# Kernel optimization log

Measured on AMD Instinct MI355X. Metric: run time of the kernel, lower is better.

The kernel has to match this reference:

```python
import jax, jax.numpy as jnp
import numpy as np

LATENT = 32
GRID = 32
G1 = GRID + 1  # 33 samples per axis (align_corners grid)
HID = 128
N_POINTS = 1048576


def _trilinear_sample(emb, points):
    """Faithful F.grid_sample(mode='bilinear', padding_mode='zeros', align_corners=True).
    emb: [(G1)^3, C] flat table; points: [n,3] in [-1,1], (x,y,z) -> (W,H,D)."""
    C = emb.shape[1]
    # torch .view(1, C, D, H, W) on the flat [(G1)^3 * C] buffer: same reshape here.
    vol = emb.reshape(C, G1, G1, G1).transpose(1, 2, 3, 0)  # [D, H, W, C]
    # align_corners=True: u in [-1,1] -> pixel coord (u+1)/2 * (size-1)
    coords = (points + 1.0) * (0.5 * (G1 - 1))
    x, y, z = coords[:, 0], coords[:, 1], coords[:, 2]
    x0 = jnp.floor(x); y0 = jnp.floor(y); z0 = jnp.floor(z)
    fx = x - x0; fy = y - y0; fz = z - z0
    x0i = x0.astype(jnp.int32); y0i = y0.astype(jnp.int32); z0i = z0.astype(jnp.int32)
    x1i = x0i + 1; y1i = y0i + 1; z1i = z0i + 1

    def corner(zi, yi, xi, w):
        valid = ((zi >= 0) & (zi < G1) & (yi >= 0) & (yi < G1)
                 & (xi >= 0) & (xi < G1))
        zc = jnp.clip(zi, 0, G1 - 1)
        yc = jnp.clip(yi, 0, G1 - 1)
        xc = jnp.clip(xi, 0, G1 - 1)
        v = vol[zc, yc, xc]  # [n, C] gather
        return v * (w * valid.astype(w.dtype))[:, None]

    wx0, wx1 = 1.0 - fx, fx
    wy0, wy1 = 1.0 - fy, fy
    wz0, wz1 = 1.0 - fz, fz
    lat = (corner(z0i, y0i, x0i, wz0 * wy0 * wx0)
           + corner(z0i, y0i, x1i, wz0 * wy0 * wx1)
           + corner(z0i, y1i, x0i, wz0 * wy1 * wx0)
           + corner(z0i, y1i, x1i, wz0 * wy1 * wx1)
           + corner(z1i, y0i, x0i, wz1 * wy0 * wx0)
           + corner(z1i, y0i, x1i, wz1 * wy0 * wx1)
           + corner(z1i, y1i, x0i, wz1 * wy1 * wx0)
           + corner(z1i, y1i, x1i, wz1 * wy1 * wx1))
    return lat  # [n, C]


def setup_inputs() -> dict:
    key = jax.random.key(0)
    ks = jax.random.split(key, 8)
    points = jax.random.uniform(ks[0], (N_POINTS, 3), dtype=jnp.float32)  # in [0,1) subset of [-1,1]
    emb = jax.random.normal(ks[1], (G1 ** 3, LATENT), dtype=jnp.float32)
    w1 = jax.random.normal(ks[2], (LATENT, HID), dtype=jnp.float32) * 0.05
    b1 = jax.random.normal(ks[3], (HID,), dtype=jnp.float32) * 0.05
    w2 = jax.random.normal(ks[4], (HID, HID), dtype=jnp.float32) * 0.05
    b2 = jax.random.normal(ks[5], (HID,), dtype=jnp.float32) * 0.05
    w3 = jax.random.normal(ks[6], (HID, 1), dtype=jnp.float32) * 0.05
    b3 = jax.random.normal(ks[7], (1,), dtype=jnp.float32) * 0.05
    return {"points": points, "emb": emb, "w1": w1, "b1": b1,
            "w2": w2, "b2": b2, "w3": w3, "b3": b3}


def reference(points, emb, w1, b1, w2, b2, w3, b3):
    lat = _trilinear_sample(emb, points)                # [n, latent]
    h = jax.nn.relu(lat @ w1 + b1)                      # [n, hid]
    h = jax.nn.relu(h @ w2 + b2)                        # [n, hid]
    sdf = jnp.tanh(h @ w3 + b3)                         # [n, 1]
    return sdf
```

## Files before the change

### kernel.cpp

```cpp
#include <hip/hip_runtime.h>
#include <hip/hip_bf16.h>

#define NPTS 1048576
#define G1I  33
#define NV   35937
#define NC   32
#define HIDD 128

typedef _Float16 h8  __attribute__((ext_vector_type(8)));
typedef _Float16 h4  __attribute__((ext_vector_type(4)));
typedef __fp16   p2  __attribute__((ext_vector_type(2)));
typedef float    f4  __attribute__((ext_vector_type(4)));

#define AS_GLOBAL(p) ((const __attribute__((address_space(1))) char*)(p))
#define AS_LDS(p)    ((__attribute__((address_space(3))) char*)(p))

#define WS_A1  0
#define WS_A2  8192
#define WS_EMB 65536
#define WS_NEED (WS_EMB + NV*NC*2)


__global__ __launch_bounds__(256) void vox_prep(
    const float* __restrict__ emb, const float* __restrict__ w1,
    const float* __restrict__ w2, char* __restrict__ ws)
{
    __shared__ _Float16 tile[256][NC];
    const int b = blockIdx.x, t = threadIdx.x;
    _Float16* embh = (_Float16*)(ws + WS_EMB);
    if (b < 141) {
        const int v = b*256 + t;
        #pragma unroll
        for (int c = 0; c < NC; ++c) {
            float val = (v < NV) ? emb[c*NV + v] : 0.f;
            tile[t][c] = (_Float16)val;
        }
        __syncthreads();
        if (v < NV) {
            uint4* dst = (uint4*)(embh + v*NC);
            const uint4* src = (const uint4*)&tile[t][0];
            #pragma unroll
            for (int j = 0; j < 4; ++j) dst[j] = src[j];
        }
    } else if (b < 149) {
        const int t2 = b - 141;
        const int ks = t >> 6, l = t & 63;
        const int gq = l >> 4, colh = l & 15;
        _Float16* a2f = (_Float16*)(ws + WS_A2);
        h8 fr;
        #pragma unroll
        for (int i = 0; i < 8; ++i) {
            const int k = 32*ks + 16*(i>>2) + 4*gq + (i&3);
            fr[i] = (_Float16)w2[k*HIDD + 16*t2 + colh];
        }
        *(h8*)(a2f + ((t2*4+ks)*64 + l)*8) = fr;
    } else {
        _Float16* a1f = (_Float16*)(ws + WS_A1);
        #pragma unroll
        for (int it = 0; it < 2; ++it) {
            const int item = t + it*256;
            const int t8 = item >> 6, l = item & 63;
            const int gq = l >> 4, colh = l & 15;
            h8 fr;
            #pragma unroll
            for (int i = 0; i < 8; ++i) {
                const int k = 16*(i>>2) + 4*gq + (i&3);
                fr[i] = (_Float16)w1[k*HIDD + 16*t8 + colh];
            }
            *(h8*)(a1f + (t8*64 + l)*8) = fr;
        }
    }
}

__global__ __launch_bounds__(256) void vox_main(
    const float* __restrict__ points, const char* __restrict__ ws,
    const float* __restrict__ b1, const float* __restrict__ b2,
    const float* __restrict__ w3, const float* __restrict__ b3v,
    float* __restrict__ out)
{
    __shared__ _Float16 latl[256][40];
    __shared__ uint4    a2l[2048];

    const int tid  = threadIdx.x;
    const int lane = tid & 63;
    const int wv   = tid >> 6;
    const int gq   = lane >> 4;
    const int colh = lane & 15;

    {
        const uint4* a2g = (const uint4*)(ws + WS_A2);
        #pragma unroll
        for (int j = 0; j < 8; ++j) {
            const uint4* gsrc = a2g + (j*256 + wv*64 + lane);
            uint4*       ldst = ((uint4*)a2l) + (j*256 + wv*64);
            __builtin_amdgcn_global_load_lds(
                (const __attribute__((address_space(1))) void*)AS_GLOBAL(gsrc),
                (__attribute__((address_space(3))) void*)AS_LDS(ldst),
                16, 0, 0);
        }
    }

    const _Float16* embh = (const _Float16*)(ws + WS_EMB);
    const int p = blockIdx.x*256 + tid;
    const float px = points[3*p+0], py = points[3*p+1], pz = points[3*p+2];
    const float xc = (px + 1.f)*16.f, yc = (py + 1.f)*16.f, zc = (pz + 1.f)*16.f;
    const float xf = floorf(xc), yf = floorf(yc), zf = floorf(zc);
    const float fx = xc - xf, fy = yc - yf, fz = zc - zf;
    const int vb = (((int)zf)*G1I + (int)yf)*G1I + (int)xf;

    const int q  = lane >> 2;
    const int ch = lane & 3;
    h8 accch[4];
    #pragma unroll
    for (int sh = 0; sh < 4; ++sh) {
        const int s = sh*16 + q;
        const float fxs = __shfl(fx, s);
        const float fys = __shfl(fy, s);
        const float fzs = __shfl(fz, s);
        const int   vbs = __shfl(vb, s);
        const float wx1 = fxs, wx0 = 1.f - fxs;
        const float wy1 = fys, wy0 = 1.f - fys;
        const float wz1 = fzs, wz0 = 1.f - fzs;
        float w8c[8];
        w8c[0] = wz0*wy0*wx0; w8c[1] = wz0*wy0*wx1;
        w8c[2] = wz0*wy1*wx0; w8c[3] = wz0*wy1*wx1;
        w8c[4] = wz1*wy0*wx0; w8c[5] = wz1*wy0*wx1;
        w8c[6] = wz1*wy1*wx0; w8c[7] = wz1*wy1*wx1;
        h8 a = (h8){0,0,0,0,0,0,0,0};
        #pragma unroll
        for (int c = 0; c < 8; ++c) {
            const int off = (c>>2)*(G1I*G1I) + ((c>>1)&1)*G1I + (c&1);
            const h8 v = *(const h8*)(embh + (vbs + off)*NC + ch*8);
            const _Float16 wh = (_Float16)w8c[c];
            const h8 wp = {wh,wh,wh,wh,wh,wh,wh,wh};
            a += wp * v;
        }
        accch[sh] = a;
    }
    #pragma unroll
    for (int sh = 0; sh < 4; ++sh)
        *(uint4*)&latl[wv*64 + sh*16 + q][8*ch] = *(uint4*)&accch[sh];
    asm volatile("s_waitcnt lgkmcnt(0)" ::: "memory");

    const h8* a1g = (const h8*)(ws + WS_A1);
    h8 a1fr[8];
    #pragma unroll
    for (int t8 = 0; t8 < 8; ++t8) a1fr[t8] = a1g[t8*64 + lane];

    h8 B2f[4][4];
    #pragma unroll
    for (int pt = 0; pt < 4; ++pt) {
        const int row = wv*64 + pt*16 + colh;
        const h4 blo = *(const h4*)&latl[row][4*gq];
        const h4 bhi = *(const h4*)&latl[row][16 + 4*gq];
        h8 bf;
        #pragma unroll
        for (int j = 0; j < 4; ++j) { bf[j] = blo[j]; bf[4+j] = bhi[j]; }
        f4 acc1[8];
        #pragma unroll
        for (int t8 = 0; t8 < 8; ++t8) acc1[t8] = *(const f4*)(b1 + 16*t8 + 4*gq);
        #pragma unroll
        for (int t8 = 0; t8 < 8; ++t8)
            acc1[t8] = __builtin_amdgcn_mfma_f32_16x16x32_f16(a1fr[t8], bf, acc1[t8], 0, 0, 0);
        #pragma unroll
        for (int ks = 0; ks < 4; ++ks) {
            union { h8 v; p2 h[4]; } u;
            const p2 z = {(__fp16)0, (__fp16)0};
            u.h[0] = __builtin_elementwise_max(__builtin_amdgcn_cvt_pkrtz(acc1[2*ks  ][0], acc1[2*ks  ][1]), z);
            u.h[1] = __builtin_elementwise_max(__builtin_amdgcn_cvt_pkrtz(acc1[2*ks  ][2], acc1[2*ks  ][3]), z);
            u.h[2] = __builtin_elementwise_max(__builtin_amdgcn_cvt_pkrtz(acc1[2*ks+1][0], acc1[2*ks+1][1]), z);
            u.h[3] = __builtin_elementwise_max(__builtin_amdgcn_cvt_pkrtz(acc1[2*ks+1][2], acc1[2*ks+1][3]), z);
            B2f[pt][ks] = u.v;
        }
    }

    asm volatile("s_waitcnt vmcnt(0)" ::: "memory");
    __syncthreads();

    float part[4] = {0.f, 0.f, 0.f, 0.f};
    #pragma unroll
    for (int t2 = 0; t2 < 8; ++t2) {
        const f4 b2q = *(const f4*)(b2 + 16*t2 + 4*gq);
        const f4 w3q = *(const f4*)(w3 + 16*t2 + 4*gq);
        f4 acc2[4];
        #pragma unroll
        for (int pt = 0; pt < 4; ++pt) acc2[pt] = b2q;
        #pragma unroll
        for (int ks = 0; ks < 4; ++ks) {
            const h8 a2fr = *(const h8*)&a2l[(t2*4 + ks)*64 + lane];
            #pragma unroll
            for (int pt = 0; pt < 4; ++pt)
                acc2[pt] = __builtin_amdgcn_mfma_f32_16x16x32_f16(a2fr, B2f[pt][ks], acc2[pt], 0, 0, 0);
        }
        #pragma unroll
        for (int pt = 0; pt < 4; ++pt)
            #pragma unroll
            for (int r = 0; r < 4; ++r)
                part[pt] += fmaxf(acc2[pt][r], 0.f) * w3q[r];
    }

    float sv = 0.f;
    #pragma unroll
    for (int pt = 0; pt < 4; ++pt) {
        float s = part[pt];
        s += __shfl_xor(s, 16);
        s += __shfl_xor(s, 32);
        if (gq == pt) sv = s;
    }
    const float zi = sv + b3v[0];
    const float e  = __expf(2.f*zi);
    out[blockIdx.x*256 + tid] = (e - 1.f) / (e + 1.f);
}

extern "C" void kernel_launch(void* const* d_in, const int* in_sizes, int n_in,
                              void* d_out, int out_size, void* d_ws, size_t ws_size,
                              hipStream_t stream)
{
    const float* points = (const float*)d_in[0];
    const float* emb    = (const float*)d_in[1];
    const float* w1     = (const float*)d_in[2];
    const float* b1     = (const float*)d_in[3];
    const float* w2     = (const float*)d_in[4];
    const float* b2     = (const float*)d_in[5];
    const float* w3     = (const float*)d_in[6];
    const float* b3     = (const float*)d_in[7];
    float* out = (float*)d_out;
    char*  ws  = (char*)d_ws;
    if (ws_size < (size_t)WS_NEED) return;

    hipLaunchKernelGGL(vox_prep, dim3(150), dim3(256), 0, stream, emb, w1, w2, ws);
    hipLaunchKernelGGL(vox_main, dim3(NPTS/256), dim3(256), 0, stream,
                       points, ws, b1, b2, w3, b3, out);
}
```

Measured before the change: 141.7 us.

## Compute final w3 projection with MFMA and hoist trilinear gathers

The final 128->1 layer becomes an MFMA: w3 is packed in the prep kernel into an fp16 A-fragment replicated across rows, and the layer-2 ReLU outputs are converted to fp16 B-fragments. This replaces the per-element scalar FMA reduction and cross-lane shuffles. The eight corner gathers are also issued up front with byte-offset addressing so more loads are in flight at once. In exchange the layer-2 activations are rounded to fp16 before the last dot product, which costs some accuracy, and more registers are live.

```diff
diff --git a/kernel.cpp b/kernel.cpp
--- a/kernel.cpp
+++ b/kernel.cpp
@@ -17,13 +17,15 @@
 
 #define WS_A1  0
 #define WS_A2  8192
+#define WS_A3  40960
 #define WS_EMB 65536
 #define WS_NEED (WS_EMB + NV*NC*2)
 
 
 __global__ __launch_bounds__(256) void vox_prep(
     const float* __restrict__ emb, const float* __restrict__ w1,
-    const float* __restrict__ w2, char* __restrict__ ws)
+    const float* __restrict__ w2, const float* __restrict__ w3,
+    char* __restrict__ ws)
 {
     __shared__ _Float16 tile[256][NC];
     const int b = blockIdx.x, t = threadIdx.x;
@@ -54,7 +56,7 @@
             fr[i] = (_Float16)w2[k*HIDD + 16*t2 + colh];
         }
         *(h8*)(a2f + ((t2*4+ks)*64 + l)*8) = fr;
-    } else {
+    } else if (b == 149) {
         _Float16* a1f = (_Float16*)(ws + WS_A1);
         #pragma unroll
         for (int it = 0; it < 2; ++it) {
@@ -69,14 +71,24 @@
             }
             *(h8*)(a1f + (t8*64 + l)*8) = fr;
         }
+    } else {
+        _Float16* a3f = (_Float16*)(ws + WS_A3);
+        const int j = t >> 6, l = t & 63;
+        const int gq = l >> 4;
+        h8 fr;
+        #pragma unroll
+        for (int i = 0; i < 8; ++i) {
+            const int k = 32*j + 16*(i>>2) + 4*gq + (i&3);
+            fr[i] = (_Float16)w3[k];
+        }
+        *(h8*)(a3f + (j*64 + l)*8) = fr;
     }
 }
 
 __global__ __launch_bounds__(256) void vox_main(
     const float* __restrict__ points, const char* __restrict__ ws,
     const float* __restrict__ b1, const float* __restrict__ b2,
-    const float* __restrict__ w3, const float* __restrict__ b3v,
-    float* __restrict__ out)
+    const float* __restrict__ b3v, float* __restrict__ out)
 {
     __shared__ _Float16 latl[256][40];
     __shared__ uint4    a2l[2048];
@@ -100,7 +112,7 @@
         }
     }
 
-    const _Float16* embh = (const _Float16*)(ws + WS_EMB);
+    const char* embB = (const char*)(ws + WS_EMB);
     const int p = blockIdx.x*256 + tid;
     const float px = points[3*p+0], py = points[3*p+1], pz = points[3*p+2];
     const float xc = (px + 1.f)*16.f, yc = (py + 1.f)*16.f, zc = (pz + 1.f)*16.f;
@@ -118,22 +130,29 @@
         const float fys = __shfl(fy, s);
         const float fzs = __shfl(fz, s);
         const int   vbs = __shfl(vb, s);
+        const char* bz0 = embB + (size_t)((unsigned)vbs*64u + (unsigned)ch*16u);
+        const char* bz1 = bz0 + 69696;
+        const h8 v0 = *(const h8*)(bz0 +    0);
+        const h8 v1 = *(const h8*)(bz0 +   64);
+        const h8 v2 = *(const h8*)(bz0 + 2112);
+        const h8 v3 = *(const h8*)(bz0 + 2176);
+        const h8 v4 = *(const h8*)(bz1 +    0);
+        const h8 v5 = *(const h8*)(bz1 +   64);
+        const h8 v6 = *(const h8*)(bz1 + 2112);
+        const h8 v7 = *(const h8*)(bz1 + 2176);
         const float wx1 = fxs, wx0 = 1.f - fxs;
         const float wy1 = fys, wy0 = 1.f - fys;
         const float wz1 = fzs, wz0 = 1.f - fzs;
-        float w8c[8];
-        w8c[0] = wz0*wy0*wx0; w8c[1] = wz0*wy0*wx1;
-        w8c[2] = wz0*wy1*wx0; w8c[3] = wz0*wy1*wx1;
-        w8c[4] = wz1*wy0*wx0; w8c[5] = wz1*wy0*wx1;
-        w8c[6] = wz1*wy1*wx0; w8c[7] = wz1*wy1*wx1;
         h8 a = (h8){0,0,0,0,0,0,0,0};
-        #pragma unroll
-        for (int c = 0; c < 8; ++c) {
-            const int off = (c>>2)*(G1I*G1I) + ((c>>1)&1)*G1I + (c&1);
-            const h8 v = *(const h8*)(embh + (vbs + off)*NC + ch*8);
-            const _Float16 wh = (_Float16)w8c[c];
-            const h8 wp = {wh,wh,wh,wh,wh,wh,wh,wh};
-            a += wp * v;
+        {
+            const _Float16 w0 = (_Float16)(wz0*wy0*wx0); const h8 W0 = {w0,w0,w0,w0,w0,w0,w0,w0}; a += W0*v0;
+            const _Float16 w1_ = (_Float16)(wz0*wy0*wx1); const h8 W1 = {w1_,w1_,w1_,w1_,w1_,w1_,w1_,w1_}; a += W1*v1;
+            const _Float16 w2_ = (_Float16)(wz0*wy1*wx0); const h8 W2 = {w2_,w2_,w2_,w2_,w2_,w2_,w2_,w2_}; a += W2*v2;
+            const _Float16 w3_ = (_Float16)(wz0*wy1*wx1); const h8 W3 = {w3_,w3_,w3_,w3_,w3_,w3_,w3_,w3_}; a += W3*v3;
+            const _Float16 w4_ = (_Float16)(wz1*wy0*wx0); const h8 W4 = {w4_,w4_,w4_,w4_,w4_,w4_,w4_,w4_}; a += W4*v4;
+            const _Float16 w5_ = (_Float16)(wz1*wy0*wx1); const h8 W5 = {w5_,w5_,w5_,w5_,w5_,w5_,w5_,w5_}; a += W5*v5;
+            const _Float16 w6_ = (_Float16)(wz1*wy1*wx0); const h8 W6 = {w6_,w6_,w6_,w6_,w6_,w6_,w6_,w6_}; a += W6*v6;
+            const _Float16 w7_ = (_Float16)(wz1*wy1*wx1); const h8 W7 = {w7_,w7_,w7_,w7_,w7_,w7_,w7_,w7_}; a += W7*v7;
         }
         accch[sh] = a;
     }
@@ -177,36 +196,47 @@
     asm volatile("s_waitcnt vmcnt(0)" ::: "memory");
     __syncthreads();
 
-    float part[4] = {0.f, 0.f, 0.f, 0.f};
-    #pragma unroll
-    for (int t2 = 0; t2 < 8; ++t2) {
-        const f4 b2q = *(const f4*)(b2 + 16*t2 + 4*gq);
-        const f4 w3q = *(const f4*)(w3 + 16*t2 + 4*gq);
-        f4 acc2[4];
-        #pragma unroll
-        for (int pt = 0; pt < 4; ++pt) acc2[pt] = b2q;
+    const h8* a3g = (const h8*)(ws + WS_A3);
+    f4 acc3[4];
+    #pragma unroll
+    for (int pt = 0; pt < 4; ++pt) acc3[pt] = (f4){0.f,0.f,0.f,0.f};
+    #pragma unroll
+    for (int q2 = 0; q2 < 4; ++q2) {
+        const f4 b2e = *(const f4*)(b2 + 16*(2*q2  ) + 4*gq);
+        const f4 b2o = *(const f4*)(b2 + 16*(2*q2+1) + 4*gq);
+        f4 acc2e[4], acc2o[4];
+        #pragma unroll
+        for (int pt = 0; pt < 4; ++pt) { acc2e[pt] = b2e; acc2o[pt] = b2o; }
         #pragma unroll
         for (int ks = 0; ks < 4; ++ks) {
-            const h8 a2fr = *(const h8*)&a2l[(t2*4 + ks)*64 + lane];
+            const h8 fe = *(const h8*)&a2l[((2*q2  )*4 + ks)*64 + lane];
             #pragma unroll
             for (int pt = 0; pt < 4; ++pt)
-                acc2[pt] = __builtin_amdgcn_mfma_f32_16x16x32_f16(a2fr, B2f[pt][ks], acc2[pt], 0, 0, 0);
-        }
-        #pragma unroll
-        for (int pt = 0; pt < 4; ++pt)
-            #pragma unroll
-            for (int r = 0; r < 4; ++r)
-                part[pt] += fmaxf(acc2[pt][r], 0.f) * w3q[r];
+                acc2e[pt] = __builtin_amdgcn_mfma_f32_16x16x32_f16(fe, B2f[pt][ks], acc2e[pt], 0, 0, 0);
+        }
+        #pragma unroll
+        for (int ks = 0; ks < 4; ++ks) {
+            const h8 fo = *(const h8*)&a2l[((2*q2+1)*4 + ks)*64 + lane];
+            #pragma unroll
+            for (int pt = 0; pt < 4; ++pt)
+                acc2o[pt] = __builtin_amdgcn_mfma_f32_16x16x32_f16(fo, B2f[pt][ks], acc2o[pt], 0, 0, 0);
+        }
+        const h8 a3fr = a3g[q2*64 + lane];
+        #pragma unroll
+        for (int pt = 0; pt < 4; ++pt) {
+            union { h8 v; p2 h[4]; } u;
+            const p2 z = {(__fp16)0, (__fp16)0};
+            u.h[0] = __builtin_elementwise_max(__builtin_amdgcn_cvt_pkrtz(acc2e[pt][0], acc2e[pt][1]), z);
+            u.h[1] = __builtin_elementwise_max(__builtin_amdgcn_cvt_pkrtz(acc2e[pt][2], acc2e[pt][3]), z);
+            u.h[2] = __builtin_elementwise_max(__builtin_amdgcn_cvt_pkrtz(acc2o[pt][0], acc2o[pt][1]), z);
+            u.h[3] = __builtin_elementwise_max(__builtin_amdgcn_cvt_pkrtz(acc2o[pt][2], acc2o[pt][3]), z);
+            acc3[pt] = __builtin_amdgcn_mfma_f32_16x16x32_f16(a3fr, u.v, acc3[pt], 0, 0, 0);
+        }
     }
 
     float sv = 0.f;
     #pragma unroll
-    for (int pt = 0; pt < 4; ++pt) {
-        float s = part[pt];
-        s += __shfl_xor(s, 16);
-        s += __shfl_xor(s, 32);
-        if (gq == pt) sv = s;
-    }
+    for (int pt = 0; pt < 4; ++pt) if (gq == pt) sv = acc3[pt][0];
     const float zi = sv + b3v[0];
     const float e  = __expf(2.f*zi);
     out[blockIdx.x*256 + tid] = (e - 1.f) / (e + 1.f);
@@ -228,7 +258,7 @@
     char*  ws  = (char*)d_ws;
     if (ws_size < (size_t)WS_NEED) return;
 
-    hipLaunchKernelGGL(vox_prep, dim3(150), dim3(256), 0, stream, emb, w1, w2, ws);
+    hipLaunchKernelGGL(vox_prep, dim3(151), dim3(256), 0, stream, emb, w1, w2, w3, ws);
     hipLaunchKernelGGL(vox_main, dim3(NPTS/256), dim3(256), 0, stream,
-                       points, ws, b1, b2, w3, b3, out);
+                       points, ws, b1, b2, b3, out);
 }
```

Result: faster. 135.2 us (-4.6%).
